# Kernel optimization log

Hardware: AMD Instinct MI355X
Metric: run time of the kernel (lower is better)

Reference implementation:

```python
import jax, jax.numpy as jnp
import numpy as np

SCALE_FACTOR = 2  # init kwarg
KERNEL = 1        # kernel=1 -> no Gaussian inpainting of empty cells
EPS = 1e-6


def token2map_agg(x, loc_orig, idx_agg, H, W):
    """Scatter-average aggregated tokens onto a dense [B,C,H,W] map.

    Faithful to token2map_agg_sparse with weight=None, kernel=1:
      each original position i gets feature x[idx_agg[i]] with weight 1,
      scattered to the grid cell of loc_orig[i]; per-cell average with
      denominator (count + 1e-6).
    """
    B, N, C = x.shape
    N0 = loc_orig.shape[1]
    lo = jnp.clip(loc_orig, -1.0, 1.0)
    wh = jnp.array([W, H], dtype=lo.dtype)
    # normalized [-1,1] -> pixel coords, round-half-even like torch.round
    px = jnp.round(0.5 * (lo + 1.0) * wh - 0.5).astype(jnp.int32)
    ix = jnp.clip(px[..., 0], 0, W - 1)
    iy = jnp.clip(px[..., 1], 0, H - 1)
    seg = (iy * W + ix + jnp.arange(B, dtype=jnp.int32)[:, None] * (H * W)).reshape(-1)  # [B*N0]
    # gather token feature for each original position: [B, N0, C]
    feats = jnp.take_along_axis(x, idx_agg[..., None].astype(jnp.int32), axis=1)
    # scatter features and counts together in one segment_sum
    src = jnp.concatenate([feats, jnp.ones_like(feats[..., :1])], axis=-1).reshape(B * N0, C + 1)
    agg = jax.ops.segment_sum(src, seg, num_segments=B * H * W)  # [B*H*W, C+1]
    out = agg[:, :C] / (agg[:, C:] + EPS)
    return out.reshape(B, H, W, C).transpose(0, 3, 1, 2)  # [B,C,H,W]


def setup_inputs() -> dict:
    key = jax.random.key(0)
    k1, k2, k3, k4 = jax.random.split(key, 4)
    B, N, C = 8, 1024, 128
    N0 = 16384  # 128*128 original grid positions
    x = jax.random.normal(k1, (B, N, C), dtype=jnp.float32)
    loc = jax.random.uniform(k2, (B, N, 2), dtype=jnp.float32, minval=-1.0, maxval=1.0)
    loc_orig = jax.random.uniform(k3, (B, N0, 2), dtype=jnp.float32, minval=-1.0, maxval=1.0)
    idx_agg = jax.random.randint(k4, (B, N0), 0, N, dtype=jnp.int32)
    return {"x": x, "loc": loc, "loc_orig": loc_orig, "idx_agg": idx_agg,
            "map_h": 128, "map_w": 128}


def reference(x, loc, loc_orig, idx_agg, map_h, map_w):
    B, N, C = x.shape
    N0 = idx_agg.shape[1]
    scale_orig = (N0 // N) ** 0.5  # static python value
    if SCALE_FACTOR <= scale_orig:
        h, w = int(map_h * SCALE_FACTOR), int(map_w * SCALE_FACTOR)
        out = token2map_agg(x, loc_orig, idx_agg, h, w)
    else:
        h, w = int(map_h * scale_orig), int(map_w * scale_orig)
        out = token2map_agg(x, loc_orig, idx_agg, h, w)
        h, w = int(map_h * SCALE_FACTOR), int(map_w * SCALE_FACTOR)
        out = jax.image.resize(out, (B, C, h, w), method="bilinear")
    return out
```

## Files before the change

kernel.cpp:

```cpp
#include <hip/hip_runtime.h>

constexpr int B  = 8;
constexpr int N  = 1024;
constexpr int C  = 128;
constexpr int N0 = 16384;
constexpr int HH = 256;
constexpr int WW = 256;
constexpr int HW = HH * WW;
constexpr int NPTS = B * N0;

constexpr int CPG  = 128;
constexpr int GPB  = HW / CPG;
constexpr int NGRP = B * GPB;
constexpr int CAP  = 96;

constexpr int SROW = CPG + 4;
constexpr int ACC_WORDS = C * SROW;
constexpr int LDS_BYTES = (ACC_WORDS + CPG + CAP) * 4;

__device__ __forceinline__ int cell_of(float lx, float ly) {
    lx = fminf(fmaxf(lx, -1.0f), 1.0f);
    ly = fminf(fmaxf(ly, -1.0f), 1.0f);
    float pxf = rintf(0.5f * (lx + 1.0f) * 256.0f - 0.5f);
    float pyf = rintf(0.5f * (ly + 1.0f) * 256.0f - 0.5f);
    int ix = (int)pxf; ix = ix < 0 ? 0 : (ix > WW - 1 ? WW - 1 : ix);
    int iy = (int)pyf; iy = iy < 0 ? 0 : (iy > HH - 1 ? HH - 1 : iy);
    return iy * WW + ix;
}

__global__ void bucket_kernel(const float* __restrict__ loc_orig,
                              const int* __restrict__ idx_agg,
                              int* __restrict__ cursor,
                              int* __restrict__ bucket) {
    int p = blockIdx.x * blockDim.x + threadIdx.x;
    if (p >= NPTS) return;
    float2 l = ((const float2*)loc_orig)[p];
    int b = p >> 14;
    int cell = cell_of(l.x, l.y);
    int g = b * GPB + (cell >> 7);
    int pos = atomicAdd(cursor + g, 1);
    if (pos < CAP) bucket[g * CAP + pos] = ((cell & 127) << 10) | idx_agg[p];
}

__global__ __launch_bounds__(256) void gather_kernel(
        const float* __restrict__ x,
        const int* __restrict__ cursor,
        const int* __restrict__ bucket,
        float* __restrict__ out) {
    extern __shared__ float smem[];
    float* acc  = smem;
    float* cntf = smem + ACC_WORDS;
    int*   recs = (int*)(cntf + CPG);

    int gid   = blockIdx.x;
    int b     = gid >> 9;
    int cell0 = (gid & 511) * CPG;
    int tid   = threadIdx.x;
    int wave  = tid >> 6, lane = tid & 63;

    float4 z4 = make_float4(0.f, 0.f, 0.f, 0.f);
    for (int i = tid; i < ACC_WORDS / 4; i += 256) ((float4*)acc)[i] = z4;
    if (tid < CPG) cntf[tid] = 0.0f;

    int cnt = cursor[gid];
    cnt = cnt > CAP ? CAP : cnt;
    if (tid < cnt) recs[tid] = bucket[gid * CAP + tid];
    __syncthreads();

    for (int j = wave; j < cnt; j += 4) {
        int e = recs[j];
        int local = e >> 10;
        int tok   = e & 1023;
        float2 v = ((const float2*)(x + (size_t)(b * N + tok) * C))[lane];
        atomicAdd(&acc[(2 * lane)     * SROW + local], v.x);
        atomicAdd(&acc[(2 * lane + 1) * SROW + local], v.y);
        if (lane == 0) atomicAdd(&cntf[local], 1.0f);
    }
    __syncthreads();
    if (tid < CPG) cntf[tid] = 1.0f / (cntf[tid] + 1e-6f);
    __syncthreads();

    int sub   = tid & 31;
    int cpick = tid >> 5;
    float s0 = cntf[4 * sub + 0];
    float s1 = cntf[4 * sub + 1];
    float s2 = cntf[4 * sub + 2];
    float s3 = cntf[4 * sub + 3];
    float* obase = out + (size_t)b * C * HW + cell0;
    #pragma unroll
    for (int it = 0; it < 16; ++it) {
        int c = it * 8 + cpick;
        float4 v = *(const float4*)&acc[c * SROW + 4 * sub];
        v.x *= s0; v.y *= s1; v.z *= s2; v.w *= s3;
        ((float4*)(obase + (size_t)c * HW))[sub] = v;
    }
}

extern "C" void kernel_launch(void* const* d_in, const int* in_sizes, int n_in,
                              void* d_out, int out_size, void* d_ws, size_t ws_size,
                              hipStream_t stream) {
    const float* x        = (const float*)d_in[0];
    const float* loc_orig = (const float*)d_in[2];
    const int*   idx_agg  = (const int*)d_in[3];
    float* out = (float*)d_out;

    int* cursor = (int*)d_ws;
    int* bucket = cursor + NGRP;

    hipMemsetAsync(cursor, 0, NGRP * sizeof(int), stream);
    bucket_kernel<<<(NPTS + 255) / 256, 256, 0, stream>>>(loc_orig, idx_agg, cursor, bucket);
    gather_kernel<<<NGRP, 256, LDS_BYTES, stream>>>(x, cursor, bucket, out);
}
```

Before: 360.6 us.

## Fuse bucketing into gather kernel by having each block scan its batch

Drops the global bucket pass, the cursor memset and the workspace buffers. Each gather block now scans every point of its batch, computes each point's cell and keeps the ones that fall in its 128-cell group in shared-memory records using LDS atomics. This removes two launches and the global atomic contention, but every block re-reads the whole batch's location array, so location reads and cell math are repeated 512-fold per batch. The record capacity also rises to 256, and counts are taken during the scan, so they include points beyond the record cap.

```diff
diff --git a/kernel.cpp b/kernel.cpp
--- a/kernel.cpp
+++ b/kernel.cpp
@@ -7,16 +7,14 @@
 constexpr int HH = 256;
 constexpr int WW = 256;
 constexpr int HW = HH * WW;
-constexpr int NPTS = B * N0;
 
 constexpr int CPG  = 128;
 constexpr int GPB  = HW / CPG;
 constexpr int NGRP = B * GPB;
-constexpr int CAP  = 96;
+constexpr int CAP  = 256;
 
 constexpr int SROW = CPG + 4;
 constexpr int ACC_WORDS = C * SROW;
-constexpr int LDS_BYTES = (ACC_WORDS + CPG + CAP) * 4;
 
 __device__ __forceinline__ int cell_of(float lx, float ly) {
     lx = fminf(fmaxf(lx, -1.0f), 1.0f);
@@ -28,44 +26,43 @@
     return iy * WW + ix;
 }
 
-__global__ void bucket_kernel(const float* __restrict__ loc_orig,
-                              const int* __restrict__ idx_agg,
-                              int* __restrict__ cursor,
-                              int* __restrict__ bucket) {
-    int p = blockIdx.x * blockDim.x + threadIdx.x;
-    if (p >= NPTS) return;
-    float2 l = ((const float2*)loc_orig)[p];
-    int b = p >> 14;
-    int cell = cell_of(l.x, l.y);
-    int g = b * GPB + (cell >> 7);
-    int pos = atomicAdd(cursor + g, 1);
-    if (pos < CAP) bucket[g * CAP + pos] = ((cell & 127) << 10) | idx_agg[p];
-}
-
-__global__ __launch_bounds__(256) void gather_kernel(
+__global__ __launch_bounds__(256) void fused_kernel(
         const float* __restrict__ x,
-        const int* __restrict__ cursor,
-        const int* __restrict__ bucket,
+        const float* __restrict__ loc_orig,
+        const int* __restrict__ idx_agg,
         float* __restrict__ out) {
-    extern __shared__ float smem[];
-    float* acc  = smem;
-    float* cntf = smem + ACC_WORDS;
-    int*   recs = (int*)(cntf + CPG);
+    __shared__ float acc[ACC_WORDS];
+    __shared__ float cntf[CPG];
+    __shared__ int   recs[CAP];
+    __shared__ int   nmatch;
 
     int gid   = blockIdx.x;
     int b     = gid >> 9;
-    int cell0 = (gid & 511) * CPG;
+    int grp   = gid & 511;
+    int cell0 = grp * CPG;
     int tid   = threadIdx.x;
     int wave  = tid >> 6, lane = tid & 63;
 
     float4 z4 = make_float4(0.f, 0.f, 0.f, 0.f);
     for (int i = tid; i < ACC_WORDS / 4; i += 256) ((float4*)acc)[i] = z4;
     if (tid < CPG) cntf[tid] = 0.0f;
+    if (tid == 0) nmatch = 0;
+    __syncthreads();
 
-    int cnt = cursor[gid];
-    cnt = cnt > CAP ? CAP : cnt;
-    if (tid < cnt) recs[tid] = bucket[gid * CAP + tid];
+    const float2* loc = (const float2*)(loc_orig) + (size_t)b * N0;
+    const int*    idx = idx_agg + (size_t)b * N0;
+    for (int p = tid; p < N0; p += 256) {
+        float2 l = loc[p];
+        int cell = cell_of(l.x, l.y);
+        if ((cell >> 7) == grp) {
+            int pos = atomicAdd(&nmatch, 1);
+            if (pos < CAP) recs[pos] = ((cell & 127) << 10) | idx[p];
+            atomicAdd(&cntf[cell & 127], 1.0f);
+        }
+    }
     __syncthreads();
+
+    int cnt = nmatch; cnt = cnt > CAP ? CAP : cnt;
 
     for (int j = wave; j < cnt; j += 4) {
         int e = recs[j];
@@ -74,7 +71,6 @@
         float2 v = ((const float2*)(x + (size_t)(b * N + tok) * C))[lane];
         atomicAdd(&acc[(2 * lane)     * SROW + local], v.x);
         atomicAdd(&acc[(2 * lane + 1) * SROW + local], v.y);
-        if (lane == 0) atomicAdd(&cntf[local], 1.0f);
     }
     __syncthreads();
     if (tid < CPG) cntf[tid] = 1.0f / (cntf[tid] + 1e-6f);
@@ -104,10 +100,5 @@
     const int*   idx_agg  = (const int*)d_in[3];
     float* out = (float*)d_out;
 
-    int* cursor = (int*)d_ws;
-    int* bucket = cursor + NGRP;
-
-    hipMemsetAsync(cursor, 0, NGRP * sizeof(int), stream);
-    bucket_kernel<<<(NPTS + 255) / 256, 256, 0, stream>>>(loc_orig, idx_agg, cursor, bucket);
-    gather_kernel<<<NGRP, 256, LDS_BYTES, stream>>>(x, cursor, bucket, out);
+    fused_kernel<<<NGRP, 256, 0, stream>>>(x, loc_orig, idx_agg, out);
 }
```

Result: slower. 580.1 us (+60.9%).
